# Performance work log

Measured on AMD Instinct MI355X. Metric: run time of the kernel, lower is better.

Reference implementation:

```python
import jax, jax.numpy as jnp
import numpy as np

N, E, H, C = 50000, 800000, 4, 32   # nodes, edges, heads, per-head channels
HID, LAT, G = H * C, 32, 128        # hidden, latent, num graphs
IN_DIM = 64
NEG_SLOPE = 0.2
BN_EPS = 1e-5


def setup_inputs() -> dict:
    key = jax.random.key(0)
    ks = jax.random.split(key, 20)
    inp = {
        "x": jax.random.normal(ks[0], (N, IN_DIM), jnp.float32),
        "edge_index": jax.random.randint(ks[1], (2, E), 0, N, jnp.int32),
        "batch": jnp.sort(jax.random.randint(ks[2], (N,), 0, G, jnp.int32)),
        # layer 0
        "W0": jax.random.normal(ks[3], (IN_DIM, HID), jnp.float32) * (1.0 / np.sqrt(IN_DIM)),
        "a_src0": jax.random.normal(ks[4], (H, C), jnp.float32) * 0.1,
        "a_dst0": jax.random.normal(ks[5], (H, C), jnp.float32) * 0.1,
        "b0": jnp.zeros((HID,), jnp.float32),
        # layer 1
        "W1": jax.random.normal(ks[6], (HID, HID), jnp.float32) * (1.0 / np.sqrt(HID)),
        "a_src1": jax.random.normal(ks[7], (H, C), jnp.float32) * 0.1,
        "a_dst1": jax.random.normal(ks[8], (H, C), jnp.float32) * 0.1,
        "b1": jnp.zeros((HID,), jnp.float32),
        # layer 2
        "W2": jax.random.normal(ks[9], (HID, HID), jnp.float32) * (1.0 / np.sqrt(HID)),
        "a_src2": jax.random.normal(ks[10], (H, C), jnp.float32) * 0.1,
        "a_dst2": jax.random.normal(ks[11], (H, C), jnp.float32) * 0.1,
        "b2": jnp.zeros((HID,), jnp.float32),
        # head
        "fc_w": jax.random.normal(ks[12], (HID, LAT), jnp.float32) * (1.0 / np.sqrt(HID)),
        "fc_b": jnp.zeros((LAT,), jnp.float32),
        "bn_g": jnp.ones((LAT,), jnp.float32),
        "bn_b": jnp.zeros((LAT,), jnp.float32),
    }
    return inp


def _gat_conv(x, src, dst, W, a_src, a_dst, b):
    n = x.shape[0]
    h = (x @ W).reshape(n, H, C)                      # [N,H,C]
    alpha_s = jnp.einsum("nhc,hc->nh", h, a_src)       # [N,H]
    alpha_d = jnp.einsum("nhc,hc->nh", h, a_dst)
    e = jax.nn.leaky_relu(alpha_s[src] + alpha_d[dst], NEG_SLOPE)  # [E',H]
    # scatter-softmax over incoming edges of each dst node
    m = jax.ops.segment_max(e, dst, num_segments=n)
    m = jnp.where(jnp.isfinite(m), m, 0.0)
    ex = jnp.exp(e - m[dst])
    denom = jax.ops.segment_sum(ex, dst, num_segments=n)
    alpha = ex / (denom[dst] + 1e-16)                  # [E',H]
    out = jax.ops.segment_sum(alpha[:, :, None] * h[src], dst, num_segments=n)
    return out.reshape(n, H * C) + b


def reference(x, edge_index, batch, W0, a_src0, a_dst0, b0, W1, a_src1, a_dst1, b1,
              W2, a_src2, a_dst2, b2, fc_w, fc_b, bn_g, bn_b):
    # PyG GATConv default add_self_loops=True
    loop = jnp.arange(N, dtype=edge_index.dtype)
    src = jnp.concatenate([edge_index[0], loop])
    dst = jnp.concatenate([edge_index[1], loop])

    h = x
    for (W, a_s, a_d, b) in ((W0, a_src0, a_dst0, b0),
                             (W1, a_src1, a_dst1, b1),
                             (W2, a_src2, a_dst2, b2)):
        h = _gat_conv(h, src, dst, W, a_s, a_d, b)
        h = jax.nn.leaky_relu(h, NEG_SLOPE)  # dropout is identity in eval

    pooled = jax.ops.segment_sum(h, batch, num_segments=G)  # global_add_pool -> [G,HID]
    out = pooled @ fc_w + fc_b
    # BatchNorm1d in eval mode with running_mean=0, running_var=1
    out = bn_g * out * (1.0 / np.sqrt(1.0 + BN_EPS)) + bn_b
    return out
```

## Files before the change

kernel.cpp:

```cpp
#include <hip/hip_runtime.h>
#include <hip/hip_bf16.h>
#include <float.h>

#define NEG 0.2f
#define SEGSHIFT 13

__device__ __forceinline__ float leaky(float x) { return x > 0.0f ? x : NEG * x; }

__device__ __forceinline__ unsigned short f2bf(float f) {
  unsigned x = __float_as_uint(f);
  unsigned r = (x + 0x7fffu + ((x >> 16) & 1u)) >> 16;
  return (unsigned short)r;
}

__device__ __forceinline__ float2 bf2f2(unsigned u) {
  float2 r;
  r.x = __uint_as_float(u << 16);
  r.y = __uint_as_float(u & 0xffff0000u);
  return r;
}

using frag8 = __attribute__((ext_vector_type(8))) short;
using f32x4v = __attribute__((ext_vector_type(4))) float;

__global__ void zero_kernel(int* __restrict__ p, int n) {
  int i = blockIdx.x * blockDim.x + threadIdx.x;
  int stride = gridDim.x * blockDim.x;
  for (; i < n; i += stride) p[i] = 0;
}

__global__ void wcvt_kernel(const float* __restrict__ W, unsigned short* __restrict__ Wt, int K) {
  int i = blockIdx.x * 256 + threadIdx.x;
  if (i >= K * 128) return;
  int k = i >> 7, n = i & 127;
  Wt[n * K + k] = f2bf(W[i]);
}

__global__ void count_kernel(const int* __restrict__ ei, int* __restrict__ degseg,
                             int E, int N, int nseg) {
  int i = blockIdx.x * blockDim.x + threadIdx.x;
  if (i >= E + N) return;
  int src, dst;
  if (i < E) { src = ei[i]; dst = ei[E + i]; } else { src = dst = i - E; }
  atomicAdd(&degseg[(size_t)dst * nseg + (src >> SEGSHIFT)], 1);
}

__global__ __launch_bounds__(1024) void scan_block_kernel(const int* __restrict__ deg,
                                                          int* __restrict__ row_start,
                                                          int* __restrict__ sums, int n) {
  __shared__ int buf[1024];
  int t = threadIdx.x;
  int idx = blockIdx.x * 1024 + t;
  int x = (idx < n) ? deg[idx] : 0;
  int v = x;
  buf[t] = v;
  __syncthreads();
  for (int off = 1; off < 1024; off <<= 1) {
    int a = (t >= off) ? buf[t - off] : 0;
    __syncthreads();
    v += a;
    buf[t] = v;
    __syncthreads();
  }
  if (idx < n) row_start[idx] = v - x;
  if (t == 1023) sums[blockIdx.x] = v;
}

__global__ __launch_bounds__(1024) void scan_sums_kernel(int* __restrict__ sums,
                                                         int* __restrict__ row_start,
                                                         int nch, int n) {
  __shared__ int buf[1024];
  int t = threadIdx.x;
  int x = (t < nch) ? sums[t] : 0;
  int v = x;
  buf[t] = v;
  __syncthreads();
  for (int off = 1; off < 1024; off <<= 1) {
    int a = (t >= off) ? buf[t - off] : 0;
    __syncthreads();
    v += a;
    buf[t] = v;
    __syncthreads();
  }
  if (t < nch) sums[t] = v - x;
  if (t == 1023) row_start[n] = v;
}

__global__ __launch_bounds__(1024) void scan_add_kernel(int* __restrict__ row_start,
                                                        const int* __restrict__ sums, int n) {
  int idx = blockIdx.x * 1024 + threadIdx.x;
  if (idx < n) row_start[idx] += sums[blockIdx.x];
}

__global__ void fill_kernel(const int* __restrict__ ei, int* __restrict__ cursor,
                            const int* __restrict__ rowseg, int* __restrict__ csr_src,
                            int E, int N, int nseg) {
  int i = blockIdx.x * blockDim.x + threadIdx.x;
  if (i >= E + N) return;
  int src, dst;
  if (i < E) { src = ei[i]; dst = ei[E + i]; } else { src = dst = i - E; }
  size_t b = (size_t)dst * nseg + (src >> SEGSHIFT);
  int pos = atomicAdd(&cursor[b], 1);
  csr_src[rowseg[b] + pos] = src;
}

template <int FP32IN>
__global__ __launch_bounds__(256) void gemm_kernel(const void* __restrict__ Xin,
                                                   const unsigned short* __restrict__ Wtg,
                                                   unsigned short* __restrict__ Hb,
                                                   const float* __restrict__ a_src,
                                                   const float* __restrict__ a_dst,
                                                   float* __restrict__ as_arr,
                                                   float* __restrict__ ad_arr,
                                                   int nrows, int K) {
  __shared__ unsigned short Wt[128][136];
  __shared__ unsigned short Xs[64][136];
  int t = threadIdx.x;
  int wave = t >> 6, lane = t & 63;
  int n0 = lane & 15, quad = lane >> 4;
  int row0 = blockIdx.x * 64, wrow = wave * 16;

  for (int idx = t; idx < (K * 128) / 8; idx += 256) {
    int n = idx / (K >> 3), c8 = idx % (K >> 3);
    *(uint4*)(&Wt[n][c8 * 8]) = *(const uint4*)(Wtg + (size_t)n * K + c8 * 8);
  }
  int rowElems = K >> 3;
  if (FP32IN) {
    const float* Xf = (const float*)Xin;
    for (int idx = t; idx < 64 * K; idx += 256) {
      int r = idx / K, k = idx % K;
      int gr = row0 + r;
      Xs[r][k] = f2bf(gr < nrows ? Xf[(size_t)gr * K + k] : 0.f);
    }
  } else {
    const unsigned short* Xb = (const unsigned short*)Xin;
    for (int idx = t; idx < 64 * rowElems; idx += 256) {
      int r = idx / rowElems, c8 = idx % rowElems;
      int gr = row0 + r;
      uint4 v = make_uint4(0, 0, 0, 0);
      if (gr < nrows) v = *(const uint4*)(Xb + (size_t)gr * K + c8 * 8);
      *(uint4*)(&Xs[r][c8 * 8]) = v;
    }
  }
  __syncthreads();

  f32x4v acc[8];
#pragma unroll
  for (int c = 0; c < 8; ++c) acc[c] = (f32x4v){0.f, 0.f, 0.f, 0.f};

  for (int kb = 0; kb < K; kb += 32) {
    frag8 a = *(const frag8*)(&Xs[wrow + n0][kb + quad * 8]);
#pragma unroll
    for (int c = 0; c < 8; ++c) {
      frag8 b = *(const frag8*)(&Wt[c * 16 + n0][kb + quad * 8]);
      acc[c] = __builtin_amdgcn_mfma_f32_16x16x32_bf16(a, b, acc[c], 0, 0, 0);
    }
  }

  float asv[8], adv[8];
#pragma unroll
  for (int c = 0; c < 8; ++c) {
    asv[c] = a_src[c * 16 + n0];
    adv[c] = a_dst[c * 16 + n0];
  }
#pragma unroll
  for (int r = 0; r < 4; ++r) {
    float ps[4] = {0.f, 0.f, 0.f, 0.f}, pd[4] = {0.f, 0.f, 0.f, 0.f};
#pragma unroll
    for (int c = 0; c < 8; ++c) {
      int h = c >> 1;
      ps[h] += acc[c][r] * asv[c];
      pd[h] += acc[c][r] * adv[c];
    }
#pragma unroll
    for (int off = 1; off < 16; off <<= 1) {
#pragma unroll
      for (int h = 0; h < 4; ++h) {
        ps[h] += __shfl_xor(ps[h], off);
        pd[h] += __shfl_xor(pd[h], off);
      }
    }
    if (n0 == 0) {
      int m = row0 + wrow + quad * 4 + r;
      if (m < nrows) {
#pragma unroll
        for (int h = 0; h < 4; ++h) {
          as_arr[(size_t)m * 4 + h] = ps[h];
          ad_arr[(size_t)m * 4 + h] = pd[h];
        }
      }
    }
  }

  __syncthreads();
#pragma unroll
  for (int c = 0; c < 8; ++c)
#pragma unroll
    for (int r = 0; r < 4; ++r)
      Xs[wrow + quad * 4 + r][c * 16 + n0] = f2bf(acc[c][r]);
  __syncthreads();
  for (int idx = t; idx < 64 * 16; idx += 256) {
    int r = idx >> 4, c8 = idx & 15;
    int gr = row0 + r;
    if (gr < nrows)
      *(uint4*)(Hb + (size_t)gr * 128 + c8 * 8) = *(const uint4*)(&Xs[r][c8 * 8]);
  }
}

template <int POOL>
__global__ __launch_bounds__(256) void agg_kernel(const unsigned short* __restrict__ Hb,
                                                  const float* __restrict__ as_arr,
                                                  const float* __restrict__ ad_arr,
                                                  const int* __restrict__ csr_src,
                                                  const int* __restrict__ rowseg,
                                                  const float* __restrict__ bias,
                                                  unsigned short* __restrict__ xnext,
                                                  const int* __restrict__ batch,
                                                  float* __restrict__ pooled,
                                                  int N, int nseg) {
  int wid = threadIdx.x >> 6;
  int lane = threadIdx.x & 63;
  int n = blockIdx.x * 4 + wid;
  if (n >= N) return;
  int rs = rowseg[(size_t)n * nseg];
  int re = rowseg[(size_t)n * nseg + nseg];
  int l16 = lane & 15;
  int sub = lane >> 4;
  int head = l16 >> 2;

  float adv = ad_arr[(size_t)n * 4 + head];
  const uint4* hb4 = (const uint4*)Hb;

  float denom = 0.f;
  float acc[8];
#pragma unroll
  for (int c = 0; c < 8; ++c) acc[c] = 0.f;

  int i = rs;
  for (; i + 8 <= re; i += 8) {
    int s0 = csr_src[i + sub];
    int s1 = csr_src[i + 4 + sub];
    float as0 = as_arr[(size_t)s0 * 4 + head];
    float as1 = as_arr[(size_t)s1 * 4 + head];
    uint4 u0 = hb4[(size_t)s0 * 16 + l16];
    uint4 u1 = hb4[(size_t)s1 * 16 + l16];
    float e0 = __expf(fminf(leaky(as0 + adv), 80.f));
    float e1 = __expf(fminf(leaky(as1 + adv), 80.f));
    denom += e0 + e1;
    float2 f;
    f = bf2f2(u0.x); acc[0] += e0 * f.x; acc[1] += e0 * f.y;
    f = bf2f2(u0.y); acc[2] += e0 * f.x; acc[3] += e0 * f.y;
    f = bf2f2(u0.z); acc[4] += e0 * f.x; acc[5] += e0 * f.y;
    f = bf2f2(u0.w); acc[6] += e0 * f.x; acc[7] += e0 * f.y;
    f = bf2f2(u1.x); acc[0] += e1 * f.x; acc[1] += e1 * f.y;
    f = bf2f2(u1.y); acc[2] += e1 * f.x; acc[3] += e1 * f.y;
    f = bf2f2(u1.z); acc[4] += e1 * f.x; acc[5] += e1 * f.y;
    f = bf2f2(u1.w); acc[6] += e1 * f.x; acc[7] += e1 * f.y;
  }
  for (; i < re; i += 4) {
    if (i + sub < re) {
      int s0 = csr_src[i + sub];
      float as0 = as_arr[(size_t)s0 * 4 + head];
      uint4 u0 = hb4[(size_t)s0 * 16 + l16];
      float e0 = __expf(fminf(leaky(as0 + adv), 80.f));
      denom += e0;
      float2 f;
      f = bf2f2(u0.x); acc[0] += e0 * f.x; acc[1] += e0 * f.y;
      f = bf2f2(u0.y); acc[2] += e0 * f.x; acc[3] += e0 * f.y;
      f = bf2f2(u0.z); acc[4] += e0 * f.x; acc[5] += e0 * f.y;
      f = bf2f2(u0.w); acc[6] += e0 * f.x; acc[7] += e0 * f.y;
    }
  }

  denom += __shfl_xor(denom, 16);
#pragma unroll
  for (int c = 0; c < 8; ++c) acc[c] += __shfl_xor(acc[c], 16);
  denom += __shfl_xor(denom, 32);
#pragma unroll
  for (int c = 0; c < 8; ++c) acc[c] += __shfl_xor(acc[c], 32);

  float inv = 1.0f / (denom + 1e-16f);
  if (POOL) {
    int g = batch[n];
    int c0 = 2 * sub;
    float v0 = leaky(acc[c0] * inv + bias[8 * l16 + c0]);
    float v1 = leaky(acc[c0 + 1] * inv + bias[8 * l16 + c0 + 1]);
    atomicAdd(&pooled[(size_t)g * 128 + 8 * l16 + c0], v0);
    atomicAdd(&pooled[(size_t)g * 128 + 8 * l16 + c0 + 1], v1);
  } else {
    if (sub == 0) {
      float4 bv0 = *(const float4*)(bias + 8 * l16);
      float4 bv1 = *(const float4*)(bias + 8 * l16 + 4);
      float v0 = leaky(acc[0] * inv + bv0.x);
      float v1 = leaky(acc[1] * inv + bv0.y);
      float v2 = leaky(acc[2] * inv + bv0.z);
      float v3 = leaky(acc[3] * inv + bv0.w);
      float v4 = leaky(acc[4] * inv + bv1.x);
      float v5 = leaky(acc[5] * inv + bv1.y);
      float v6 = leaky(acc[6] * inv + bv1.z);
      float v7 = leaky(acc[7] * inv + bv1.w);
      uint4 pk;
      pk.x = ((unsigned)f2bf(v1) << 16) | (unsigned)f2bf(v0);
      pk.y = ((unsigned)f2bf(v3) << 16) | (unsigned)f2bf(v2);
      pk.z = ((unsigned)f2bf(v5) << 16) | (unsigned)f2bf(v4);
      pk.w = ((unsigned)f2bf(v7) << 16) | (unsigned)f2bf(v6);
      ((uint4*)xnext)[(size_t)n * 16 + l16] = pk;
    }
  }
}

__global__ void head_kernel(const float* __restrict__ pooled, const float* __restrict__ fc_w,
                            const float* __restrict__ fc_b, const float* __restrict__ bn_g,
                            const float* __restrict__ bn_b, float* __restrict__ out, int G) {
  int t = threadIdx.x;
  int g = blockIdx.x * 8 + (t >> 5);
  int j = t & 31;
  if (g >= G) return;
  const float* pr = pooled + (size_t)g * 128;
  float acc = 0.f;
#pragma unroll 8
  for (int k = 0; k < 128; ++k) acc += pr[k] * fc_w[k * 32 + j];
  const float inv = 0.9999950000374997f;
  out[g * 32 + j] = bn_g[j] * (acc + fc_b[j]) * inv + bn_b[j];
}

extern "C" void kernel_launch(void* const* d_in, const int* in_sizes, int n_in,
                              void* d_out, int out_size, void* d_ws, size_t ws_size,
                              hipStream_t stream) {
  const float* x = (const float*)d_in[0];
  const int* ei = (const int*)d_in[1];
  const int* batch = (const int*)d_in[2];
  const float* Wm[3] = {(const float*)d_in[3], (const float*)d_in[7], (const float*)d_in[11]};
  const float* a_s[3] = {(const float*)d_in[4], (const float*)d_in[8], (const float*)d_in[12]};
  const float* a_d[3] = {(const float*)d_in[5], (const float*)d_in[9], (const float*)d_in[13]};
  const float* bb[3] = {(const float*)d_in[6], (const float*)d_in[10], (const float*)d_in[14]};
  const float* fc_w = (const float*)d_in[15];
  const float* fc_b = (const float*)d_in[16];
  const float* bn_g = (const float*)d_in[17];
  const float* bn_b = (const float*)d_in[18];
  float* out = (float*)d_out;

  int N = in_sizes[0] / 64;
  int E = in_sizes[1] / 2;
  int G = out_size / 32;
  int Etot = E + N;
  int nseg = ((N - 1) >> SEGSHIFT) + 1;
  int L = N * nseg;

  char* p = (char*)d_ws;
  auto carve = [&](size_t bytes) {
    char* r = p;
    p += (bytes + 255) & ~size_t(255);
    return r;
  };
  int* degseg    = (int*)carve((size_t)L * 4);
  int* cursor    = (int*)carve((size_t)L * 4);
  float* pooled  = (float*)carve((size_t)G * 128 * 4);
  int* rowseg    = (int*)carve((size_t)(L + 1) * 4);
  int* sums      = (int*)carve(4096);
  int* csr_src   = (int*)carve((size_t)Etot * 4);
  unsigned short* Hb  = (unsigned short*)carve((size_t)N * 128 * 2);
  unsigned short* Xb  = (unsigned short*)carve((size_t)N * 128 * 2);
  unsigned short* Wt0 = (unsigned short*)carve(64 * 128 * 2);
  unsigned short* Wt1 = (unsigned short*)carve(128 * 128 * 2);
  unsigned short* Wt2 = (unsigned short*)carve(128 * 128 * 2);
  float* as_arr  = (float*)carve((size_t)N * 4 * 4);
  float* ad_arr  = (float*)carve((size_t)N * 4 * 4);

  int nz = (int)(((char*)(pooled + (size_t)G * 128) - (char*)degseg) / 4);
  zero_kernel<<<512, 256, 0, stream>>>(degseg, nz);

  wcvt_kernel<<<(64 * 128 + 255) / 256, 256, 0, stream>>>(Wm[0], Wt0, 64);
  wcvt_kernel<<<(128 * 128 + 255) / 256, 256, 0, stream>>>(Wm[1], Wt1, 128);
  wcvt_kernel<<<(128 * 128 + 255) / 256, 256, 0, stream>>>(Wm[2], Wt2, 128);

  int egrid = (Etot + 255) / 256;
  count_kernel<<<egrid, 256, 0, stream>>>(ei, degseg, E, N, nseg);
  int nch = (L + 1023) / 1024;
  scan_block_kernel<<<nch, 1024, 0, stream>>>(degseg, rowseg, sums, L);
  scan_sums_kernel<<<1, 1024, 0, stream>>>(sums, rowseg, nch, L);
  scan_add_kernel<<<nch, 1024, 0, stream>>>(rowseg, sums, L);
  fill_kernel<<<egrid, 256, 0, stream>>>(ei, cursor, rowseg, csr_src, E, N, nseg);

  int ggrid = (N + 63) / 64;
  int ngrid = (N + 3) / 4;

  gemm_kernel<1><<<ggrid, 256, 0, stream>>>(x, Wt0, Hb, a_s[0], a_d[0], as_arr, ad_arr, N, 64);
  agg_kernel<0><<<ngrid, 256, 0, stream>>>(Hb, as_arr, ad_arr, csr_src, rowseg, bb[0],
                                           Xb, nullptr, nullptr, N, nseg);
  gemm_kernel<0><<<ggrid, 256, 0, stream>>>(Xb, Wt1, Hb, a_s[1], a_d[1], as_arr, ad_arr, N, 128);
  agg_kernel<0><<<ngrid, 256, 0, stream>>>(Hb, as_arr, ad_arr, csr_src, rowseg, bb[1],
                                           Xb, nullptr, nullptr, N, nseg);
  gemm_kernel<0><<<ggrid, 256, 0, stream>>>(Xb, Wt2, Hb, a_s[2], a_d[2], as_arr, ad_arr, N, 128);
  agg_kernel<1><<<ngrid, 256, 0, stream>>>(Hb, as_arr, ad_arr, csr_src, rowseg, bb[2],
                                           nullptr, batch, pooled, N, nseg);

  head_kernel<<<(G + 7) / 8, 256, 0, stream>>>(pooled, fc_w, fc_b, bn_g, bn_b, out, G);
}
```

Baseline: 436.7 us.

## Stage edge sources and attention weights in LDS per wavefront chunk

The aggregation kernel now loads up to 64 edge sources per wavefront in one step, one edge per lane. Each lane computes the exponentiated attention scores for all four heads with a single float4 load and stages them in shared memory. The feature-gather loop then reads source indices and weights from LDS. Before, 16 lanes each reloaded the same index and score and recomputed the same exp. The softmax denominator becomes a full-wave butterfly reduction over four heads, which adds shuffles and relies on LDS writes being visible within the wavefront without a barrier.

```diff
diff --git a/kernel.cpp b/kernel.cpp
--- a/kernel.cpp
+++ b/kernel.cpp
@@ -218,68 +218,75 @@
                                                   const int* __restrict__ batch,
                                                   float* __restrict__ pooled,
                                                   int N, int nseg) {
+  __shared__ int s_lds[4][64];
+  __shared__ float e_lds[4][4][64];
   int wid = threadIdx.x >> 6;
   int lane = threadIdx.x & 63;
   int n = blockIdx.x * 4 + wid;
   if (n >= N) return;
   int rs = rowseg[(size_t)n * nseg];
   int re = rowseg[(size_t)n * nseg + nseg];
+  int deg = re - rs;
   int l16 = lane & 15;
   int sub = lane >> 4;
   int head = l16 >> 2;
 
-  float adv = ad_arr[(size_t)n * 4 + head];
+  float4 ad4 = *(const float4*)(ad_arr + (size_t)n * 4);
   const uint4* hb4 = (const uint4*)Hb;
 
-  float denom = 0.f;
+  float4 dsum = make_float4(0.f, 0.f, 0.f, 0.f);
   float acc[8];
 #pragma unroll
   for (int c = 0; c < 8; ++c) acc[c] = 0.f;
 
-  int i = rs;
-  for (; i + 8 <= re; i += 8) {
-    int s0 = csr_src[i + sub];
-    int s1 = csr_src[i + 4 + sub];
-    float as0 = as_arr[(size_t)s0 * 4 + head];
-    float as1 = as_arr[(size_t)s1 * 4 + head];
-    uint4 u0 = hb4[(size_t)s0 * 16 + l16];
-    uint4 u1 = hb4[(size_t)s1 * 16 + l16];
-    float e0 = __expf(fminf(leaky(as0 + adv), 80.f));
-    float e1 = __expf(fminf(leaky(as1 + adv), 80.f));
-    denom += e0 + e1;
-    float2 f;
-    f = bf2f2(u0.x); acc[0] += e0 * f.x; acc[1] += e0 * f.y;
-    f = bf2f2(u0.y); acc[2] += e0 * f.x; acc[3] += e0 * f.y;
-    f = bf2f2(u0.z); acc[4] += e0 * f.x; acc[5] += e0 * f.y;
-    f = bf2f2(u0.w); acc[6] += e0 * f.x; acc[7] += e0 * f.y;
-    f = bf2f2(u1.x); acc[0] += e1 * f.x; acc[1] += e1 * f.y;
-    f = bf2f2(u1.y); acc[2] += e1 * f.x; acc[3] += e1 * f.y;
-    f = bf2f2(u1.z); acc[4] += e1 * f.x; acc[5] += e1 * f.y;
-    f = bf2f2(u1.w); acc[6] += e1 * f.x; acc[7] += e1 * f.y;
-  }
-  for (; i < re; i += 4) {
-    if (i + sub < re) {
-      int s0 = csr_src[i + sub];
-      float as0 = as_arr[(size_t)s0 * 4 + head];
-      uint4 u0 = hb4[(size_t)s0 * 16 + l16];
-      float e0 = __expf(fminf(leaky(as0 + adv), 80.f));
-      denom += e0;
+  for (int base = 0; base < deg; base += 64) {
+    int cnt = min(64, deg - base);
+    int s = 0;
+    float4 e4 = make_float4(0.f, 0.f, 0.f, 0.f);
+    if (lane < cnt) {
+      s = csr_src[rs + base + lane];
+      float4 a4 = *(const float4*)(as_arr + (size_t)s * 4);
+      e4.x = __expf(fminf(leaky(a4.x + ad4.x), 80.f));
+      e4.y = __expf(fminf(leaky(a4.y + ad4.y), 80.f));
+      e4.z = __expf(fminf(leaky(a4.z + ad4.z), 80.f));
+      e4.w = __expf(fminf(leaky(a4.w + ad4.w), 80.f));
+    }
+    dsum.x += e4.x; dsum.y += e4.y; dsum.z += e4.z; dsum.w += e4.w;
+    s_lds[wid][lane] = s;
+    e_lds[wid][0][lane] = e4.x;
+    e_lds[wid][1][lane] = e4.y;
+    e_lds[wid][2][lane] = e4.z;
+    e_lds[wid][3][lane] = e4.w;
+
+#pragma unroll 4
+    for (int j = 0; j < cnt; j += 4) {
+      int jj = j + sub;
+      float ej = e_lds[wid][head][jj];
+      int sj = s_lds[wid][jj];
+      uint4 u = hb4[(size_t)sj * 16 + l16];
       float2 f;
-      f = bf2f2(u0.x); acc[0] += e0 * f.x; acc[1] += e0 * f.y;
-      f = bf2f2(u0.y); acc[2] += e0 * f.x; acc[3] += e0 * f.y;
-      f = bf2f2(u0.z); acc[4] += e0 * f.x; acc[5] += e0 * f.y;
-      f = bf2f2(u0.w); acc[6] += e0 * f.x; acc[7] += e0 * f.y;
-    }
-  }
-
-  denom += __shfl_xor(denom, 16);
+      f = bf2f2(u.x); acc[0] += ej * f.x; acc[1] += ej * f.y;
+      f = bf2f2(u.y); acc[2] += ej * f.x; acc[3] += ej * f.y;
+      f = bf2f2(u.z); acc[4] += ej * f.x; acc[5] += ej * f.y;
+      f = bf2f2(u.w); acc[6] += ej * f.x; acc[7] += ej * f.y;
+    }
+  }
+
 #pragma unroll
   for (int c = 0; c < 8; ++c) acc[c] += __shfl_xor(acc[c], 16);
-  denom += __shfl_xor(denom, 32);
 #pragma unroll
   for (int c = 0; c < 8; ++c) acc[c] += __shfl_xor(acc[c], 32);
 
+#pragma unroll
+  for (int off = 1; off < 64; off <<= 1) {
+    dsum.x += __shfl_xor(dsum.x, off);
+    dsum.y += __shfl_xor(dsum.y, off);
+    dsum.z += __shfl_xor(dsum.z, off);
+    dsum.w += __shfl_xor(dsum.w, off);
+  }
+  float denom = (head == 0) ? dsum.x : (head == 1) ? dsum.y : (head == 2) ? dsum.z : dsum.w;
   float inv = 1.0f / (denom + 1e-16f);
+
   if (POOL) {
     int g = batch[n];
     int c0 = 2 * sub;
```

Result: slower. 471.0 us (+7.9%).

## Remap aggregation lanes to 8 edges per step and software-pipeline gather loads

Applied to the files above, without the earlier changes.

The edge-aggregation kernel now assigns 8 lanes per source row, each holding 16 channels as two uint4 loads, so a wavefront handles 8 edges per iteration instead of 4x2. The loop is software-pipelined: the next group's index, attention score and features are loaded before the current group is accumulated, hiding gather latency. Launch bounds request 6 blocks per CU to cap register use. The cost is a third cross-lane reduction stage, more accumulator registers, and a switch to select pooled outputs.

```diff
diff --git a/kernel.cpp b/kernel.cpp
--- a/kernel.cpp
+++ b/kernel.cpp
@@ -207,107 +207,148 @@
   }
 }
 
+#define LOADG(S, A, U0, U1, base)                              \
+  do {                                                         \
+    (S) = csr_src[(base) + sub];                               \
+    (A) = as_arr[(size_t)(S) * 4 + h];                         \
+    (U0) = hb4[(size_t)(S) * 16 + 2 * l8];                     \
+    (U1) = hb4[(size_t)(S) * 16 + 2 * l8 + 1];                 \
+  } while (0)
+
+#define COMPG(A, U0, U1)                                       \
+  do {                                                         \
+    float e_ = __expf(fminf(leaky((A) + adv), 80.f));          \
+    denom += e_;                                               \
+    float2 f_;                                                 \
+    f_ = bf2f2((U0).x); acc[0] += e_ * f_.x; acc[1] += e_ * f_.y;   \
+    f_ = bf2f2((U0).y); acc[2] += e_ * f_.x; acc[3] += e_ * f_.y;   \
+    f_ = bf2f2((U0).z); acc[4] += e_ * f_.x; acc[5] += e_ * f_.y;   \
+    f_ = bf2f2((U0).w); acc[6] += e_ * f_.x; acc[7] += e_ * f_.y;   \
+    f_ = bf2f2((U1).x); acc[8] += e_ * f_.x; acc[9] += e_ * f_.y;   \
+    f_ = bf2f2((U1).y); acc[10] += e_ * f_.x; acc[11] += e_ * f_.y; \
+    f_ = bf2f2((U1).z); acc[12] += e_ * f_.x; acc[13] += e_ * f_.y; \
+    f_ = bf2f2((U1).w); acc[14] += e_ * f_.x; acc[15] += e_ * f_.y; \
+  } while (0)
+
 template <int POOL>
-__global__ __launch_bounds__(256) void agg_kernel(const unsigned short* __restrict__ Hb,
-                                                  const float* __restrict__ as_arr,
-                                                  const float* __restrict__ ad_arr,
-                                                  const int* __restrict__ csr_src,
-                                                  const int* __restrict__ rowseg,
-                                                  const float* __restrict__ bias,
-                                                  unsigned short* __restrict__ xnext,
-                                                  const int* __restrict__ batch,
-                                                  float* __restrict__ pooled,
-                                                  int N, int nseg) {
+__global__ __launch_bounds__(256, 6) void agg_kernel(const unsigned short* __restrict__ Hb,
+                                                     const float* __restrict__ as_arr,
+                                                     const float* __restrict__ ad_arr,
+                                                     const int* __restrict__ csr_src,
+                                                     const int* __restrict__ rowseg,
+                                                     const float* __restrict__ bias,
+                                                     unsigned short* __restrict__ xnext,
+                                                     const int* __restrict__ batch,
+                                                     float* __restrict__ pooled,
+                                                     int N, int nseg) {
   int wid = threadIdx.x >> 6;
   int lane = threadIdx.x & 63;
   int n = blockIdx.x * 4 + wid;
   if (n >= N) return;
   int rs = rowseg[(size_t)n * nseg];
   int re = rowseg[(size_t)n * nseg + nseg];
-  int l16 = lane & 15;
-  int sub = lane >> 4;
-  int head = l16 >> 2;
-
-  float adv = ad_arr[(size_t)n * 4 + head];
+  int l8 = lane & 7;
+  int sub = lane >> 3;
+  int h = l8 >> 1;
+
+  float adv = ad_arr[(size_t)n * 4 + h];
   const uint4* hb4 = (const uint4*)Hb;
 
   float denom = 0.f;
-  float acc[8];
-#pragma unroll
-  for (int c = 0; c < 8; ++c) acc[c] = 0.f;
+  float acc[16];
+#pragma unroll
+  for (int c = 0; c < 16; ++c) acc[c] = 0.f;
 
   int i = rs;
-  for (; i + 8 <= re; i += 8) {
-    int s0 = csr_src[i + sub];
-    int s1 = csr_src[i + 4 + sub];
-    float as0 = as_arr[(size_t)s0 * 4 + head];
-    float as1 = as_arr[(size_t)s1 * 4 + head];
-    uint4 u0 = hb4[(size_t)s0 * 16 + l16];
-    uint4 u1 = hb4[(size_t)s1 * 16 + l16];
-    float e0 = __expf(fminf(leaky(as0 + adv), 80.f));
-    float e1 = __expf(fminf(leaky(as1 + adv), 80.f));
-    denom += e0 + e1;
-    float2 f;
-    f = bf2f2(u0.x); acc[0] += e0 * f.x; acc[1] += e0 * f.y;
-    f = bf2f2(u0.y); acc[2] += e0 * f.x; acc[3] += e0 * f.y;
-    f = bf2f2(u0.z); acc[4] += e0 * f.x; acc[5] += e0 * f.y;
-    f = bf2f2(u0.w); acc[6] += e0 * f.x; acc[7] += e0 * f.y;
-    f = bf2f2(u1.x); acc[0] += e1 * f.x; acc[1] += e1 * f.y;
-    f = bf2f2(u1.y); acc[2] += e1 * f.x; acc[3] += e1 * f.y;
-    f = bf2f2(u1.z); acc[4] += e1 * f.x; acc[5] += e1 * f.y;
-    f = bf2f2(u1.w); acc[6] += e1 * f.x; acc[7] += e1 * f.y;
-  }
-  for (; i < re; i += 4) {
-    if (i + sub < re) {
-      int s0 = csr_src[i + sub];
-      float as0 = as_arr[(size_t)s0 * 4 + head];
-      uint4 u0 = hb4[(size_t)s0 * 16 + l16];
-      float e0 = __expf(fminf(leaky(as0 + adv), 80.f));
-      denom += e0;
-      float2 f;
-      f = bf2f2(u0.x); acc[0] += e0 * f.x; acc[1] += e0 * f.y;
-      f = bf2f2(u0.y); acc[2] += e0 * f.x; acc[3] += e0 * f.y;
-      f = bf2f2(u0.z); acc[4] += e0 * f.x; acc[5] += e0 * f.y;
-      f = bf2f2(u0.w); acc[6] += e0 * f.x; acc[7] += e0 * f.y;
-    }
-  }
-
+  int sA;
+  float aA;
+  uint4 uA0, uA1;
+  if (i + 8 <= re) {
+    LOADG(sA, aA, uA0, uA1, i);
+    i += 8;
+    for (; i + 8 <= re; i += 8) {
+      int sB;
+      float aB;
+      uint4 uB0, uB1;
+      LOADG(sB, aB, uB0, uB1, i);
+      COMPG(aA, uA0, uA1);
+      sA = sB; aA = aB; uA0 = uB0; uA1 = uB1;
+    }
+    COMPG(aA, uA0, uA1);
+  }
+  if (i + sub < re) {
+    LOADG(sA, aA, uA0, uA1, i);
+    COMPG(aA, uA0, uA1);
+  }
+
+#pragma unroll
+  for (int c = 0; c < 16; ++c) acc[c] += __shfl_xor(acc[c], 8);
+  denom += __shfl_xor(denom, 8);
+#pragma unroll
+  for (int c = 0; c < 16; ++c) acc[c] += __shfl_xor(acc[c], 16);
   denom += __shfl_xor(denom, 16);
 #pragma unroll
-  for (int c = 0; c < 8; ++c) acc[c] += __shfl_xor(acc[c], 16);
+  for (int c = 0; c < 16; ++c) acc[c] += __shfl_xor(acc[c], 32);
   denom += __shfl_xor(denom, 32);
-#pragma unroll
-  for (int c = 0; c < 8; ++c) acc[c] += __shfl_xor(acc[c], 32);
 
   float inv = 1.0f / (denom + 1e-16f);
   if (POOL) {
     int g = batch[n];
-    int c0 = 2 * sub;
-    float v0 = leaky(acc[c0] * inv + bias[8 * l16 + c0]);
-    float v1 = leaky(acc[c0 + 1] * inv + bias[8 * l16 + c0 + 1]);
-    atomicAdd(&pooled[(size_t)g * 128 + 8 * l16 + c0], v0);
-    atomicAdd(&pooled[(size_t)g * 128 + 8 * l16 + c0 + 1], v1);
+    float p0 = 0.f, p1 = 0.f;
+    switch (sub) {
+      case 0: p0 = acc[0];  p1 = acc[1];  break;
+      case 1: p0 = acc[2];  p1 = acc[3];  break;
+      case 2: p0 = acc[4];  p1 = acc[5];  break;
+      case 3: p0 = acc[6];  p1 = acc[7];  break;
+      case 4: p0 = acc[8];  p1 = acc[9];  break;
+      case 5: p0 = acc[10]; p1 = acc[11]; break;
+      case 6: p0 = acc[12]; p1 = acc[13]; break;
+      case 7: p0 = acc[14]; p1 = acc[15]; break;
+    }
+    int ch = 16 * l8 + 2 * sub;
+    float v0 = leaky(p0 * inv + bias[ch]);
+    float v1 = leaky(p1 * inv + bias[ch + 1]);
+    atomicAdd(&pooled[(size_t)g * 128 + ch], v0);
+    atomicAdd(&pooled[(size_t)g * 128 + ch + 1], v1);
   } else {
     if (sub == 0) {
-      float4 bv0 = *(const float4*)(bias + 8 * l16);
-      float4 bv1 = *(const float4*)(bias + 8 * l16 + 4);
-      float v0 = leaky(acc[0] * inv + bv0.x);
-      float v1 = leaky(acc[1] * inv + bv0.y);
-      float v2 = leaky(acc[2] * inv + bv0.z);
-      float v3 = leaky(acc[3] * inv + bv0.w);
-      float v4 = leaky(acc[4] * inv + bv1.x);
-      float v5 = leaky(acc[5] * inv + bv1.y);
-      float v6 = leaky(acc[6] * inv + bv1.z);
-      float v7 = leaky(acc[7] * inv + bv1.w);
-      uint4 pk;
-      pk.x = ((unsigned)f2bf(v1) << 16) | (unsigned)f2bf(v0);
-      pk.y = ((unsigned)f2bf(v3) << 16) | (unsigned)f2bf(v2);
-      pk.z = ((unsigned)f2bf(v5) << 16) | (unsigned)f2bf(v4);
-      pk.w = ((unsigned)f2bf(v7) << 16) | (unsigned)f2bf(v6);
-      ((uint4*)xnext)[(size_t)n * 16 + l16] = pk;
-    }
-  }
-}
+      float4 b0 = *(const float4*)(bias + 16 * l8);
+      float4 b1 = *(const float4*)(bias + 16 * l8 + 4);
+      float4 b2 = *(const float4*)(bias + 16 * l8 + 8);
+      float4 b3 = *(const float4*)(bias + 16 * l8 + 12);
+      float v0 = leaky(acc[0] * inv + b0.x);
+      float v1 = leaky(acc[1] * inv + b0.y);
+      float v2 = leaky(acc[2] * inv + b0.z);
+      float v3 = leaky(acc[3] * inv + b0.w);
+      float v4 = leaky(acc[4] * inv + b1.x);
+      float v5 = leaky(acc[5] * inv + b1.y);
+      float v6 = leaky(acc[6] * inv + b1.z);
+      float v7 = leaky(acc[7] * inv + b1.w);
+      float v8 = leaky(acc[8] * inv + b2.x);
+      float v9 = leaky(acc[9] * inv + b2.y);
+      float v10 = leaky(acc[10] * inv + b2.z);
+      float v11 = leaky(acc[11] * inv + b2.w);
+      float v12 = leaky(acc[12] * inv + b3.x);
+      float v13 = leaky(acc[13] * inv + b3.y);
+      float v14 = leaky(acc[14] * inv + b3.z);
+      float v15 = leaky(acc[15] * inv + b3.w);
+      uint4 pk0, pk1;
+      pk0.x = ((unsigned)f2bf(v1) << 16) | (unsigned)f2bf(v0);
+      pk0.y = ((unsigned)f2bf(v3) << 16) | (unsigned)f2bf(v2);
+      pk0.z = ((unsigned)f2bf(v5) << 16) | (unsigned)f2bf(v4);
+      pk0.w = ((unsigned)f2bf(v7) << 16) | (unsigned)f2bf(v6);
+      pk1.x = ((unsigned)f2bf(v9) << 16) | (unsigned)f2bf(v8);
+      pk1.y = ((unsigned)f2bf(v11) << 16) | (unsigned)f2bf(v10);
+      pk1.z = ((unsigned)f2bf(v13) << 16) | (unsigned)f2bf(v12);
+      pk1.w = ((unsigned)f2bf(v15) << 16) | (unsigned)f2bf(v14);
+      ((uint4*)xnext)[(size_t)n * 16 + 2 * l8] = pk0;
+      ((uint4*)xnext)[(size_t)n * 16 + 2 * l8 + 1] = pk1;
+    }
+  }
+}
+
+#undef LOADG
+#undef COMPG
 
 __global__ void head_kernel(const float* __restrict__ pooled, const float* __restrict__ fc_w,
                             const float* __restrict__ fc_b, const float* __restrict__ bn_g,
```

Result: slower. 453.3 us (+3.8%).
